# Optimization experiments

Measured on AMD Instinct MI355X. Metric: run time of the kernel, lower is better.

The kernel has to match this reference:

```python
import jax, jax.numpy as jnp
import numpy as np

B = 4096      # batch of edges
D = 512       # high-dim feature size
E_DIM = 2     # visualization embedding dim
G = 1024      # number of unique edge_from rows (groups)
BIG = 1e9     # padding value pushed to end of sorts
LAMBD = 1.0
EPS = 1e-12


def setup_inputs() -> dict:
    key = jax.random.key(0)
    ks = jax.random.split(key, 7)
    pool = jax.random.normal(ks[0], (G, D), jnp.float32)
    gid = jax.random.randint(ks[1], (B,), 0, G)
    edge_from = pool[gid]  # duplicated rows -> groups, as the module expects
    edge_to = jax.random.normal(ks[2], (B, D), jnp.float32)
    embedding_to = jax.random.normal(ks[3], (B, E_DIM), jnp.float32)
    embedding_from = jax.random.normal(ks[4], (B, E_DIM), jnp.float32)
    recon_to = jax.random.normal(ks[5], (B, D), jnp.float32)
    recon_from = jax.random.normal(ks[6], (B, D), jnp.float32)
    return {
        "edge_to": edge_to, "edge_from": edge_from,
        "embedding_to": embedding_to, "embedding_from": embedding_from,
        "recon_to": recon_to, "recon_from": recon_from,
    }


def _pairwise_dist(x):
    # Euclidean pairwise distances via Gram matrix; safe sqrt (clip handles
    # rounding-negative values and the exact-zero diagonal).
    n = jnp.sum(x * x, axis=-1)
    d2 = n[:, None] + n[None, :] - 2.0 * (x @ x.T)
    return jnp.sqrt(jnp.clip(d2, EPS, None))


def batch_ranking_loss(edge_from, edge_to, embedding_from, embedding_to):
    b = edge_from.shape[0]
    # Group membership: rows of edge_from that are identical (squared distance 0).
    ef = jax.lax.stop_gradient(edge_from)
    n = jnp.sum(ef * ef, axis=-1)
    d2f = n[:, None] + n[None, :] - 2.0 * (ef @ ef.T)
    same = d2f < 1e-3                       # [B, B] bool, includes diagonal
    k = jnp.sum(same, axis=-1)              # group size per anchor row
    rep = jnp.argmax(same, axis=-1)         # first member index = group id

    d_high = jnp.where(same, _pairwise_dist(edge_to), BIG)
    d_low = jnp.where(same, _pairwise_dist(embedding_to), BIG)

    order = jnp.argsort(d_high, axis=-1)                      # rank by high-dim dist
    gathered = jnp.take_along_axis(d_low, order, axis=-1)     # low-dim dists in high order
    s = jnp.sort(gathered, axis=-1)                           # ascending; BIG pads at end
    diffs = jax.nn.relu(s[:, 1:] - s[:, :-1])                 # [B, B-1]
    pos = jnp.arange(b - 1)
    valid = pos[None, :] < (k[:, None] - 1)                   # only real-member diffs
    row = jnp.sum(jnp.where(valid, diffs, 0.0), axis=-1) / jnp.maximum(k - 1, 1)

    # Average rows within each group, then average over groups with >= 2 members.
    sum_r = jax.ops.segment_sum(row, rep, num_segments=b)
    cnt = jax.ops.segment_sum(jnp.ones((b,), row.dtype), rep, num_segments=b)
    is_group = cnt >= 2.0
    group_loss = jnp.where(is_group, sum_r / jnp.maximum(cnt, 1.0), 0.0)
    n_valid = jnp.sum(is_group.astype(row.dtype))
    return jnp.sum(group_loss) / jnp.maximum(n_valid, 1.0)


def _umap_loss(embedding_to, embedding_from):
    # Stand-in attraction term: mean log(1 + ||e_to - e_from||^2).
    d2 = jnp.sum((embedding_to - embedding_from) ** 2, axis=-1)
    return jnp.mean(jnp.log1p(d2))


def _recon_loss(edge_to, edge_from, recon_to, recon_from):
    return jnp.mean((recon_to - edge_to) ** 2) + jnp.mean((recon_from - edge_from) ** 2)


def reference(edge_to, edge_from, embedding_to, embedding_from, recon_to, recon_from):
    umap_l = _umap_loss(embedding_to, embedding_from)
    recon_l = _recon_loss(edge_to, edge_from, recon_to, recon_from)
    rank_l = batch_ranking_loss(edge_from, edge_to, embedding_from, embedding_to)
    total = umap_l + LAMBD * recon_l + rank_l
    return (umap_l, recon_l, rank_l, total)
```

## Files before the change

### kernel.cpp

```cpp
#include <hip/hip_runtime.h>
#include <stdint.h>

#define NB 4096
#define ND 512
#define K1_GRID 1024
#define TBL 4096
#define MAXK 32
#define K2_GRID (TBL / 4)
#define BLK 256

static_assert(K1_GRID * 4 == NB, "one edge_from row per wave");

static constexpr float kEps = 1e-12f;

__device__ inline uint64_t splitmix64(uint64_t x) {
    x += 0x9E3779B97F4A7C15ULL;
    x = (x ^ (x >> 30)) * 0xBF58476D1CE4E5B9ULL;
    x = (x ^ (x >> 27)) * 0x94D049BB133111EBULL;
    return x ^ (x >> 31);
}

__global__ __launch_bounds__(BLK) void k_pre(
        const float4* __restrict__ edge_to4,
        const float*  __restrict__ edge_from,
        const float2* __restrict__ emb_to,
        const float2* __restrict__ emb_from,
        const float4* __restrict__ recon_to4,
        const float*  __restrict__ recon_from,
        unsigned long long* __restrict__ tableH,
        unsigned int* __restrict__ gcount,
        int* __restrict__ gmember,
        float* __restrict__ recon_part,
        float* __restrict__ umap_part,
        unsigned int* __restrict__ counter)
{
    const int tid  = threadIdx.x;
    const int b    = blockIdx.x;
    const int wave = tid >> 6, lane = tid & 63;

    if (b == 0 && tid == 0) atomicExch(counter, 0u);

    const int row = b * 4 + wave;
    const uint4*  ef4 = reinterpret_cast<const uint4*>(edge_from  + (size_t)row * ND);
    const float4* rf4 = reinterpret_cast<const float4*>(recon_from + (size_t)row * ND);
    uint4  ua = ef4[lane * 2], ub = ef4[lane * 2 + 1];
    float4 ra = rf4[lane * 2], rb = rf4[lane * 2 + 1];
    uint32_t wbits[8] = {ua.x, ua.y, ua.z, ua.w, ub.x, ub.y, ub.z, ub.w};
    float    rvals[8] = {ra.x, ra.y, ra.z, ra.w, rb.x, rb.y, rb.z, rb.w};
    uint64_t h = 0;
    float    s = 0.f;
    const int base = lane * 8;
    #pragma unroll
    for (int t = 0; t < 8; ++t) {
        h += splitmix64((uint64_t)wbits[t] ^ ((uint64_t)(base + t) * 0xA24BAED4963EE407ULL));
        float d = rvals[t] - __uint_as_float(wbits[t]);
        s = fmaf(d, d, s);
    }
    {
        const int i0 = b * 512 + tid;
        #pragma unroll
        for (int q = 0; q < 2; ++q) {
            const int i = i0 + q * 256;
            float4 a = edge_to4[i], c = recon_to4[i];
            float t1;
            t1 = c.x - a.x; s = fmaf(t1, t1, s);
            t1 = c.y - a.y; s = fmaf(t1, t1, s);
            t1 = c.z - a.z; s = fmaf(t1, t1, s);
            t1 = c.w - a.w; s = fmaf(t1, t1, s);
        }
    }
    float uml = 0.f;
    if (tid < 4) {
        const int i = b * 4 + tid;
        float2 a = emb_to[i], c = emb_from[i];
        float dx = a.x - c.x, dy = a.y - c.y;
        uml = log1pf(fmaf(dx, dx, dy * dy));
    }
    #pragma unroll
    for (int off = 32; off; off >>= 1) h += __shfl_down(h, off, 64);
    if (lane == 0) {
        unsigned long long hh = (unsigned long long)h;
        unsigned slot = (unsigned)hh & (TBL - 1);
        while (true) {
            unsigned long long prev = atomicCAS(&tableH[slot], 0ULL, hh);
            if (prev == 0ULL || prev == hh) break;
            slot = (slot + 1) & (TBL - 1);
        }
        unsigned pos = atomicAdd(&gcount[slot], 1u);
        if (pos < MAXK) gmember[slot * MAXK + pos] = row;
    }
    #pragma unroll
    for (int off = 32; off; off >>= 1) s += __shfl_down(s, off, 64);
    if (wave == 0) {
        uml += __shfl_down(uml, 2, 64);
        uml += __shfl_down(uml, 1, 64);
    }
    __shared__ float sws[4];
    if (lane == 0) sws[wave] = s;
    __syncthreads();
    if (tid == 0) {
        recon_part[b] = sws[0] + sws[1] + sws[2] + sws[3];
        umap_part[b]  = uml;
    }
}

__global__ __launch_bounds__(BLK) void k_rank_fin(
        const unsigned int* __restrict__ gcount,
        const int* __restrict__ gmember,
        const float2* __restrict__ emb,
        const float* __restrict__ recon_part,
        const float* __restrict__ umap_part,
        float* __restrict__ vpart,
        float* __restrict__ npart,
        unsigned int* __restrict__ counter,
        float* __restrict__ out)
{
    const int tid = threadIdx.x;
    const int wave = tid >> 6, lane = tid & 63;
    const int slot = blockIdx.x * 4 + wave;

    const unsigned k = gcount[slot];
    float v = 0.f, nvf = 0.f;
    if (k >= 2u) {
        const int kk = (int)min(k, (unsigned)MAXK);
        const bool act = lane < kk;
        int myrow = act ? gmember[slot * MAXK + lane] : 0x7FFFFFFF;
        int rnk = 0;
        for (int j = 0; j < kk; ++j) {
            int rj = __shfl(myrow, j, 64);
            if (act && rj < myrow) ++rnk;
        }
        int srow = 0x7FFFFFFF;
        for (int j = 0; j < kk; ++j) {
            int rj = __shfl(myrow, j, 64);
            int pj = __shfl(rnk, j, 64);
            if (pj == lane) srow = rj;
        }
        float ex = 0.f, ey = 0.f;
        if (act) { float2 e = emb[srow]; ex = e.x; ey = e.y; }
        float d2max = -1.f, d2min = 1e30f;
        for (int j = 0; j < kk; ++j) {
            float xj = __shfl(ex, j, 64), yj = __shfl(ey, j, 64);
            float dx = ex - xj, dy = ey - yj;
            float d2 = fmaf(dx, dx, dy * dy);
            d2max = fmaxf(d2max, d2);
            d2min = fminf(d2min, d2);
        }
        float row_i = 0.f;
        if (act) {
            const float dmax = sqrtf(fmaxf(d2max, kEps));
            const float dmin = sqrtf(fmaxf(d2min, kEps));
            row_i = (dmax - dmin) / (float)(k - 1u);
        }
        #pragma unroll
        for (int off = 32; off; off >>= 1) row_i += __shfl_down(row_i, off, 64);
        if (lane == 0) { v = row_i / (float)k; nvf = 1.f; }
    }
    __shared__ float svw[4], snw[4];
    if (lane == 0) { svw[wave] = v; snw[wave] = nvf; }
    __syncthreads();
    __shared__ bool is_last;
    if (tid == 0) {
        vpart[blockIdx.x] = svw[0] + svw[1] + svw[2] + svw[3];
        npart[blockIdx.x] = snw[0] + snw[1] + snw[2] + snw[3];
        __threadfence();
        unsigned int t = atomicAdd(counter, 1u);
        is_last = (t == K2_GRID - 1);
    }
    __syncthreads();
    if (!is_last) return;
    __threadfence();

    double r = 0.0, u = 0.0, vv = 0.0, nv = 0.0;
    for (int i = tid; i < K1_GRID; i += BLK) { r += (double)recon_part[i];
                                               u += (double)umap_part[i]; }
    for (int i = tid; i < K2_GRID; i += BLK) { vv += (double)vpart[i];
                                               nv += (double)npart[i]; }
    #pragma unroll
    for (int off = 32; off; off >>= 1) {
        r  += __shfl_down(r, off, 64);  u  += __shfl_down(u, off, 64);
        vv += __shfl_down(vv, off, 64); nv += __shfl_down(nv, off, 64);
    }
    __shared__ double sr[4], su[4], sv[4], sn[4];
    const int lane2 = tid & 63, wid = tid >> 6;
    if (lane2 == 0) { sr[wid] = r; su[wid] = u; sv[wid] = vv; sn[wid] = nv; }
    __syncthreads();
    if (tid == 0) {
        double R = sr[0] + sr[1] + sr[2] + sr[3];
        double U = su[0] + su[1] + su[2] + su[3];
        double V = sv[0] + sv[1] + sv[2] + sv[3];
        double N = sn[0] + sn[1] + sn[2] + sn[3];
        double umap  = U / (double)NB;
        double recon = R / ((double)NB * (double)ND);
        double rank  = V / (N > 1.0 ? N : 1.0);
        out[0] = (float)umap;
        out[1] = (float)recon;
        out[2] = (float)rank;
        out[3] = (float)(umap + recon + rank);
    }
}

extern "C" void kernel_launch(void* const* d_in, const int* in_sizes, int n_in,
                              void* d_out, int out_size, void* d_ws, size_t ws_size,
                              hipStream_t stream) {
    const float4* edge_to4   = (const float4*)d_in[0];
    const float*  edge_from  = (const float*)d_in[1];
    const float2* emb_to     = (const float2*)d_in[2];
    const float2* emb_from   = (const float2*)d_in[3];
    const float4* recon_to4  = (const float4*)d_in[4];
    const float*  recon_from = (const float*)d_in[5];

    char* ws = (char*)d_ws;
    unsigned long long* tableH = (unsigned long long*)ws;  ws += (size_t)TBL * 8;
    unsigned int* gcount       = (unsigned int*)ws;        ws += (size_t)TBL * 4;
    int*          gmember      = (int*)ws;                 ws += (size_t)TBL * MAXK * 4;
    float*        recon_part   = (float*)ws;               ws += (size_t)K1_GRID * 4;
    float*        umap_part    = (float*)ws;               ws += (size_t)K1_GRID * 4;
    float*        vpart        = (float*)ws;               ws += (size_t)K2_GRID * 4;
    float*        npart        = (float*)ws;               ws += (size_t)K2_GRID * 4;
    unsigned int* counter      = (unsigned int*)ws;

    hipMemsetAsync(tableH, 0, (size_t)TBL * 8 + (size_t)TBL * 4, stream);

    k_pre<<<K1_GRID, BLK, 0, stream>>>(
        edge_to4, edge_from, emb_to, emb_from, recon_to4, recon_from,
        tableH, gcount, gmember, recon_part, umap_part, counter);
    k_rank_fin<<<K2_GRID, BLK, 0, stream>>>(
        gcount, gmember, emb_to, recon_part, umap_part,
        vpart, npart, counter, (float*)d_out);
}
```

Before: 40.41 us.

## Move group hash table into single-block LDS kernel and drop memset

The first kernel now only writes a per-row hash instead of inserting into a global hash table with atomics. A single 1024-thread block builds the hash table in shared memory, prefix-sums group counts into a compact member list, computes per-group ranking terms, and does the final reduction. This removes the memset launch, the global atomics and the last-block counter. In exchange, all ranking work is serialized onto one CU, which risks a longer tail. Groups are now capped at 64 members instead of 32.

```diff
diff --git a/kernel.cpp b/kernel.cpp
--- a/kernel.cpp
+++ b/kernel.cpp
@@ -5,8 +5,6 @@
 #define ND 512
 #define K1_GRID 1024
 #define TBL 4096
-#define MAXK 32
-#define K2_GRID (TBL / 4)
 #define BLK 256
 
 static_assert(K1_GRID * 4 == NB, "one edge_from row per wave");
@@ -27,18 +25,13 @@
         const float2* __restrict__ emb_from,
         const float4* __restrict__ recon_to4,
         const float*  __restrict__ recon_from,
-        unsigned long long* __restrict__ tableH,
-        unsigned int* __restrict__ gcount,
-        int* __restrict__ gmember,
+        uint64_t* __restrict__ hash,
         float* __restrict__ recon_part,
-        float* __restrict__ umap_part,
-        unsigned int* __restrict__ counter)
+        float* __restrict__ umap_part)
 {
     const int tid  = threadIdx.x;
     const int b    = blockIdx.x;
     const int wave = tid >> 6, lane = tid & 63;
-
-    if (b == 0 && tid == 0) atomicExch(counter, 0u);
 
     const int row = b * 4 + wave;
     const uint4*  ef4 = reinterpret_cast<const uint4*>(edge_from  + (size_t)row * ND);
@@ -78,17 +71,7 @@
     }
     #pragma unroll
     for (int off = 32; off; off >>= 1) h += __shfl_down(h, off, 64);
-    if (lane == 0) {
-        unsigned long long hh = (unsigned long long)h;
-        unsigned slot = (unsigned)hh & (TBL - 1);
-        while (true) {
-            unsigned long long prev = atomicCAS(&tableH[slot], 0ULL, hh);
-            if (prev == 0ULL || prev == hh) break;
-            slot = (slot + 1) & (TBL - 1);
-        }
-        unsigned pos = atomicAdd(&gcount[slot], 1u);
-        if (pos < MAXK) gmember[slot * MAXK + pos] = row;
-    }
+    if (lane == 0) hash[row] = h;
     #pragma unroll
     for (int off = 32; off; off >>= 1) s += __shfl_down(s, off, 64);
     if (wave == 0) {
@@ -104,27 +87,87 @@
     }
 }
 
-__global__ __launch_bounds__(BLK) void k_rank_fin(
-        const unsigned int* __restrict__ gcount,
-        const int* __restrict__ gmember,
+__global__ __launch_bounds__(1024) void k_single(
+        const uint64_t* __restrict__ hash,
         const float2* __restrict__ emb,
         const float* __restrict__ recon_part,
         const float* __restrict__ umap_part,
-        float* __restrict__ vpart,
-        float* __restrict__ npart,
-        unsigned int* __restrict__ counter,
         float* __restrict__ out)
 {
-    const int tid = threadIdx.x;
+    __shared__ unsigned long long tH[TBL];
+    __shared__ unsigned gcnt[TBL];
+    __shared__ unsigned gbase[TBL];
+    __shared__ int      mlist[NB];
+    __shared__ unsigned wtot[16];
+    __shared__ float    wv[16], wn[16];
+    __shared__ double   sr[16], su[16];
+
+    const int tid  = threadIdx.x;
     const int wave = tid >> 6, lane = tid & 63;
-    const int slot = blockIdx.x * 4 + wave;
-
-    const unsigned k = gcount[slot];
-    float v = 0.f, nvf = 0.f;
-    if (k >= 2u) {
-        const int kk = (int)min(k, (unsigned)MAXK);
+
+    #pragma unroll
+    for (int q = 0; q < 4; ++q) { tH[tid + q * 1024] = 0ULL; gcnt[tid + q * 1024] = 0u; }
+    __syncthreads();
+
+    int      slots[4];
+    unsigned poss[4];
+    #pragma unroll
+    for (int q = 0; q < 4; ++q) {
+        const int r = tid + q * 1024;
+        unsigned long long h = (unsigned long long)hash[r];
+        unsigned s = (unsigned)h & (TBL - 1);
+        while (true) {
+            unsigned long long prev = atomicCAS(&tH[s], 0ULL, h);
+            if (prev == 0ULL || prev == h) break;
+            s = (s + 1) & (TBL - 1);
+        }
+        slots[q] = (int)s;
+        poss[q]  = atomicAdd(&gcnt[s], 1u);
+    }
+    __syncthreads();
+
+    const unsigned x0 = gcnt[tid * 4], x1 = gcnt[tid * 4 + 1];
+    const unsigned x2 = gcnt[tid * 4 + 2], x3 = gcnt[tid * 4 + 3];
+    const unsigned tot = x0 + x1 + x2 + x3;
+    unsigned inc = tot;
+    #pragma unroll
+    for (int off = 1; off < 64; off <<= 1) {
+        unsigned n = __shfl_up(inc, off, 64);
+        if (lane >= off) inc += n;
+    }
+    if (lane == 63) wtot[wave] = inc;
+    __syncthreads();
+    if (tid < 16) {
+        unsigned mine = wtot[tid];
+        unsigned winc = mine;
+        #pragma unroll
+        for (int off = 1; off < 16; off <<= 1) {
+            unsigned n = __shfl_up(winc, off, 64);
+            if (tid >= off) winc += n;
+        }
+        wtot[tid] = winc - mine;
+    }
+    __syncthreads();
+    const unsigned ex = wtot[wave] + inc - tot;
+    gbase[tid * 4]     = ex;
+    gbase[tid * 4 + 1] = ex + x0;
+    gbase[tid * 4 + 2] = ex + x0 + x1;
+    gbase[tid * 4 + 3] = ex + x0 + x1 + x2;
+    __syncthreads();
+
+    #pragma unroll
+    for (int q = 0; q < 4; ++q)
+        mlist[gbase[slots[q]] + poss[q]] = tid + q * 1024;
+    __syncthreads();
+
+    float vsum = 0.f, nvs = 0.f;
+    for (int slot = wave; slot < TBL; slot += 16) {
+        const unsigned k = gcnt[slot];
+        if (k < 2u) continue;
+        const int kk = (int)min(k, 64u);
+        const unsigned bs = gbase[slot];
         const bool act = lane < kk;
-        int myrow = act ? gmember[slot * MAXK + lane] : 0x7FFFFFFF;
+        int myrow = act ? mlist[bs + lane] : 0x7FFFFFFF;
         int rnk = 0;
         for (int j = 0; j < kk; ++j) {
             int rj = __shfl(myrow, j, 64);
@@ -136,12 +179,12 @@
             int pj = __shfl(rnk, j, 64);
             if (pj == lane) srow = rj;
         }
-        float ex = 0.f, ey = 0.f;
-        if (act) { float2 e = emb[srow]; ex = e.x; ey = e.y; }
+        float exx = 0.f, eyy = 0.f;
+        if (act) { float2 e = emb[srow]; exx = e.x; eyy = e.y; }
         float d2max = -1.f, d2min = 1e30f;
         for (int j = 0; j < kk; ++j) {
-            float xj = __shfl(ex, j, 64), yj = __shfl(ey, j, 64);
-            float dx = ex - xj, dy = ey - yj;
+            float xj = __shfl(exx, j, 64), yj = __shfl(eyy, j, 64);
+            float dx = exx - xj, dy = eyy - yj;
             float d2 = fmaf(dx, dx, dy * dy);
             d2max = fmaxf(d2max, d2);
             d2min = fminf(d2min, d2);
@@ -154,42 +197,26 @@
         }
         #pragma unroll
         for (int off = 32; off; off >>= 1) row_i += __shfl_down(row_i, off, 64);
-        if (lane == 0) { v = row_i / (float)k; nvf = 1.f; }
-    }
-    __shared__ float svw[4], snw[4];
-    if (lane == 0) { svw[wave] = v; snw[wave] = nvf; }
-    __syncthreads();
-    __shared__ bool is_last;
+        if (lane == 0) { vsum += row_i / (float)k; nvs += 1.f; }
+    }
+    if (lane == 0) { wv[wave] = vsum; wn[wave] = nvs; }
+
+    double r = (double)recon_part[tid];
+    double u = (double)umap_part[tid];
+    #pragma unroll
+    for (int off = 32; off; off >>= 1) {
+        r += __shfl_down(r, off, 64);
+        u += __shfl_down(u, off, 64);
+    }
+    if (lane == 0) { sr[wave] = r; su[wave] = u; }
+    __syncthreads();
     if (tid == 0) {
-        vpart[blockIdx.x] = svw[0] + svw[1] + svw[2] + svw[3];
-        npart[blockIdx.x] = snw[0] + snw[1] + snw[2] + snw[3];
-        __threadfence();
-        unsigned int t = atomicAdd(counter, 1u);
-        is_last = (t == K2_GRID - 1);
-    }
-    __syncthreads();
-    if (!is_last) return;
-    __threadfence();
-
-    double r = 0.0, u = 0.0, vv = 0.0, nv = 0.0;
-    for (int i = tid; i < K1_GRID; i += BLK) { r += (double)recon_part[i];
-                                               u += (double)umap_part[i]; }
-    for (int i = tid; i < K2_GRID; i += BLK) { vv += (double)vpart[i];
-                                               nv += (double)npart[i]; }
-    #pragma unroll
-    for (int off = 32; off; off >>= 1) {
-        r  += __shfl_down(r, off, 64);  u  += __shfl_down(u, off, 64);
-        vv += __shfl_down(vv, off, 64); nv += __shfl_down(nv, off, 64);
-    }
-    __shared__ double sr[4], su[4], sv[4], sn[4];
-    const int lane2 = tid & 63, wid = tid >> 6;
-    if (lane2 == 0) { sr[wid] = r; su[wid] = u; sv[wid] = vv; sn[wid] = nv; }
-    __syncthreads();
-    if (tid == 0) {
-        double R = sr[0] + sr[1] + sr[2] + sr[3];
-        double U = su[0] + su[1] + su[2] + su[3];
-        double V = sv[0] + sv[1] + sv[2] + sv[3];
-        double N = sn[0] + sn[1] + sn[2] + sn[3];
+        double R = 0, U = 0, V = 0, N = 0;
+        #pragma unroll
+        for (int w2 = 0; w2 < 16; ++w2) {
+            R += sr[w2]; U += su[w2];
+            V += (double)wv[w2]; N += (double)wn[w2];
+        }
         double umap  = U / (double)NB;
         double recon = R / ((double)NB * (double)ND);
         double rank  = V / (N > 1.0 ? N : 1.0);
@@ -211,21 +238,13 @@
     const float*  recon_from = (const float*)d_in[5];
 
     char* ws = (char*)d_ws;
-    unsigned long long* tableH = (unsigned long long*)ws;  ws += (size_t)TBL * 8;
-    unsigned int* gcount       = (unsigned int*)ws;        ws += (size_t)TBL * 4;
-    int*          gmember      = (int*)ws;                 ws += (size_t)TBL * MAXK * 4;
-    float*        recon_part   = (float*)ws;               ws += (size_t)K1_GRID * 4;
-    float*        umap_part    = (float*)ws;               ws += (size_t)K1_GRID * 4;
-    float*        vpart        = (float*)ws;               ws += (size_t)K2_GRID * 4;
-    float*        npart        = (float*)ws;               ws += (size_t)K2_GRID * 4;
-    unsigned int* counter      = (unsigned int*)ws;
-
-    hipMemsetAsync(tableH, 0, (size_t)TBL * 8 + (size_t)TBL * 4, stream);
+    uint64_t* hash       = (uint64_t*)ws;  ws += (size_t)NB * 8;
+    float*    recon_part = (float*)ws;     ws += (size_t)K1_GRID * 4;
+    float*    umap_part  = (float*)ws;
 
     k_pre<<<K1_GRID, BLK, 0, stream>>>(
         edge_to4, edge_from, emb_to, emb_from, recon_to4, recon_from,
-        tableH, gcount, gmember, recon_part, umap_part, counter);
-    k_rank_fin<<<K2_GRID, BLK, 0, stream>>>(
-        gcount, gmember, emb_to, recon_part, umap_part,
-        vpart, npart, counter, (float*)d_out);
-}
+        hash, recon_part, umap_part);
+    k_single<<<1, 1024, 0, stream>>>(
+        hash, emb_to, recon_part, umap_part, (float*)d_out);
+}
```

Result: slower. 126.1 us (+212.1%).
